# Kernel tuning notes

Hardware: AMD Instinct MI355X
Metric: run time of the kernel (lower is better)

The kernel has to match this reference:

```python
import jax, jax.numpy as jnp
import numpy as np

DIM = 256
HEADS = 8
HEAD_DIM = DIM // HEADS            # 32
EXP_HEADS = 16                     # int(2.0 * HEADS)
N = 2048
E = 32768
SCALE = HEAD_DIM ** -0.5
MASK_VALUE = -1e9  # safe stand-in for -finfo.max (avoids inf after the head-expand linear)


def setup_inputs() -> dict:
    key = jax.random.key(0)
    ks = jax.random.split(key, 9)
    s = 0.05
    return {
        "x": jax.random.normal(ks[0], (N, DIM), dtype=jnp.float32),
        "edges": jax.random.normal(ks[1], (N, DIM), dtype=jnp.float32),
        "edge_index": jax.random.randint(ks[2], (2, E), 0, N, dtype=jnp.int64),
        "Wq": jax.random.normal(ks[3], (DIM, DIM), dtype=jnp.float32) * s,
        "Wk": jax.random.normal(ks[4], (DIM, DIM), dtype=jnp.float32) * s,
        "Wv": jax.random.normal(ks[5], (EXP_HEADS * HEAD_DIM, DIM), dtype=jnp.float32) * s,
        "Wev": jax.random.normal(ks[6], (EXP_HEADS * HEAD_DIM, DIM), dtype=jnp.float32) * s,
        "Wexp": jax.random.normal(ks[7], (EXP_HEADS, HEADS), dtype=jnp.float32) * s,
        "Wout": jax.random.normal(ks[8], (DIM, EXP_HEADS * HEAD_DIM), dtype=jnp.float32) * s,
    }


def reference(x, edges, edge_index, Wq, Wk, Wv, Wev, Wexp, Wout):
    n = x.shape[0]
    # projections; torch Linear weight is (out, in) -> x @ W.T
    q = (x @ Wq.T).reshape(n, HEADS, HEAD_DIM).transpose(1, 0, 2)            # h n d
    k = (x @ Wk.T).reshape(n, HEADS, HEAD_DIM).transpose(1, 0, 2) * SCALE    # h n d
    v = (x @ Wv.T).reshape(n, EXP_HEADS, HEAD_DIM).transpose(1, 0, 2)        # e n d
    edge_v = (edges @ Wev.T).reshape(n, EXP_HEADS, HEAD_DIM).transpose(1, 0, 2)

    src, dst = edge_index[0], edge_index[1]
    # per-edge elementwise dot product: gather q at src, k at dst
    ew = jnp.einsum('hpd,hpd->hp', q[:, src], k[:, dst])                     # h E

    # scatter into dense (heads, n, n) attention, masked elsewhere
    attn = jnp.full((HEADS, n, n), MASK_VALUE, dtype=x.dtype)
    attn = attn.at[:, src, dst].set(ew)

    # head-expand linear over the head axis: (n m h) @ (exp h)^T -> exp n m
    attn = jnp.einsum('hnm,eh->enm', attn, Wexp)
    attn = jax.nn.softmax(attn, axis=-1)

    # graph Laplacian: I - A
    attn = jnp.eye(n, dtype=x.dtype)[None, :, :] - attn                      # e n m

    vv = v + edge_v                                                          # e n d
    out = jnp.einsum('enm,emd->end', attn, vv)                               # e n d
    out = out.transpose(1, 0, 2).reshape(n, EXP_HEADS * HEAD_DIM)
    out = out @ Wout.T                                                       # n dim
    return out
```

## Files before the change

kernel.cpp:

```cpp
#include <hip/hip_runtime.h>

#define NN 2048
#define DIMM 256
#define HEADS 8
#define HEAD_DIM 32
#define EXPH 16
#define E_EDGES 32768
#define VDIM 512
#define PW 1024
#define SCALE_F 0.17677669529663687f
#define MASKV -1.0e9f
#define SLOTW 64
#define CS_BLOCKS 128
#define CS_ROWS (NN / CS_BLOCKS)

typedef __attribute__((ext_vector_type(8))) short short8;
typedef __attribute__((ext_vector_type(4))) float f32x4;

__device__ __forceinline__ unsigned short f2bf(float f) {
    unsigned int u = __float_as_uint(f);
    unsigned int r = (u + 0x7FFFu + ((u >> 16) & 1u)) >> 16;
    return (unsigned short)r;
}
__device__ __forceinline__ float bflo(unsigned int u) { return __uint_as_float(u << 16); }
__device__ __forceinline__ float bfhi(unsigned int u) { return __uint_as_float(u & 0xFFFF0000u); }

__device__ __forceinline__ int load_edge(const int* __restrict__ ei32, int is64, int idx) {
    return is64 ? ei32[2 * idx] : ei32[idx];
}

__global__ __launch_bounds__(256) void convert_init_kernel(
    const float* __restrict__ x, const float* __restrict__ edges,
    const float* __restrict__ Wq, const float* __restrict__ Wk,
    const float* __restrict__ Wv, const float* __restrict__ Wev,
    const float* __restrict__ Wout,
    unsigned short* __restrict__ xb, unsigned short* __restrict__ eb,
    unsigned short* __restrict__ Wqb, unsigned short* __restrict__ Wkb,
    unsigned short* __restrict__ Wvb, unsigned short* __restrict__ Wevb,
    unsigned short* __restrict__ Woutb,
    int* __restrict__ slotCnt)
{
    int b = blockIdx.x;
    int t = threadIdx.x;
    if (b >= 1536) {
        slotCnt[(b - 1536) * 256 + t] = 0;
        return;
    }
    int idx = b * 256 + t;
    const float* src; unsigned short* dst; int loc;
    if      (idx < 131072) { src = x;     dst = xb;    loc = idx; }
    else if (idx < 262144) { src = edges; dst = eb;    loc = idx - 131072; }
    else if (idx < 278528) { src = Wq;    dst = Wqb;   loc = idx - 262144; }
    else if (idx < 294912) { src = Wk;    dst = Wkb;   loc = idx - 278528; }
    else if (idx < 327680) { src = Wv;    dst = Wvb;   loc = idx - 294912; }
    else if (idx < 360448) { src = Wev;   dst = Wevb;  loc = idx - 327680; }
    else                   { src = Wout;  dst = Woutb; loc = idx - 360448; }
    float4 v = *(const float4*)(src + (size_t)loc * 4);
    ushort4 o;
    o.x = f2bf(v.x); o.y = f2bf(v.y); o.z = f2bf(v.z); o.w = f2bf(v.w);
    *(ushort4*)(dst + (size_t)loc * 4) = o;
}

__global__ __launch_bounds__(256) void proj_mfma_kernel(
    const unsigned short* __restrict__ xb, const unsigned short* __restrict__ eb,
    const unsigned short* __restrict__ Wqb, const unsigned short* __restrict__ Wkb,
    const unsigned short* __restrict__ Wvb, const unsigned short* __restrict__ Wevb,
    unsigned short* __restrict__ Pb)
{
    int t = threadIdx.x;
    int lane = t & 63;
    int wave = t >> 6;
    int wm = wave >> 1;
    int wn = wave & 1;
    int rowT = blockIdx.x * 32;
    int jb = blockIdx.y;
    int colT = jb * 64;

    const unsigned short* Wb; int wbase; int nseg = 1;
    if (jb < 4)      { Wb = Wqb; wbase = jb * 64; }
    else if (jb < 8) { Wb = Wkb; wbase = (jb - 4) * 64; }
    else             { Wb = Wvb; wbase = (jb - 8) * 64; nseg = 2; }

    int arow = rowT + wm * 16 + (lane & 15);
    int koff = (lane >> 4) * 8;

    f32x4 acc0 = {0.f, 0.f, 0.f, 0.f};
    f32x4 acc1 = {0.f, 0.f, 0.f, 0.f};

    for (int seg = 0; seg < nseg; ++seg) {
        const unsigned short* Ab = (seg == 0) ? xb : eb;
        const unsigned short* Wm = (seg == 0) ? Wb : Wevb;
        const unsigned short* ap  = Ab + (size_t)arow * DIMM + koff;
        const unsigned short* b0p = Wm + (size_t)(wbase + wn * 32 + (lane & 15)) * DIMM + koff;
        const unsigned short* b1p = b0p + 16 * DIMM;
        #pragma unroll
        for (int ks = 0; ks < 8; ks++) {
            short8 af = *(const short8*)(ap  + ks * 32);
            short8 b0 = *(const short8*)(b0p + ks * 32);
            short8 b1 = *(const short8*)(b1p + ks * 32);
            acc0 = __builtin_amdgcn_mfma_f32_16x16x32_bf16(af, b0, acc0, 0, 0, 0);
            acc1 = __builtin_amdgcn_mfma_f32_16x16x32_bf16(af, b1, acc1, 0, 0, 0);
        }
    }
    float sc = (jb >= 4 && jb < 8) ? SCALE_F : 1.0f;
    int crow0 = rowT + wm * 16 + (lane >> 4) * 4;
    int ccol  = colT + wn * 32 + (lane & 15);
    #pragma unroll
    for (int r = 0; r < 4; r++) {
        Pb[(size_t)(crow0 + r) * PW + ccol]      = f2bf(acc0[r] * sc);
        Pb[(size_t)(crow0 + r) * PW + ccol + 16] = f2bf(acc1[r] * sc);
    }
}

__global__ __launch_bounds__(256) void colsum1_scatter_kernel(
    const unsigned short* __restrict__ Pb, float* __restrict__ partial,
    const int* __restrict__ ei32, int* __restrict__ slotCnt,
    unsigned int* __restrict__ slots)
{
    int b = blockIdx.x;
    int t = threadIdx.x;
    int nz = __syncthreads_count(ei32[2 * t + 1] != 0);
    int is64 = (nz == 0);
    int p = b * 256 + t;
    int s = load_edge(ei32, is64, p);
    int d = load_edge(ei32, is64, E_EDGES + p);
    int pos = atomicAdd(&slotCnt[s], 1);
    if (pos < SLOTW)
        slots[(size_t)s * SLOTW + pos] = (unsigned int)(p * 2048 + d);
    int r0 = b * CS_ROWS;
    float sx = 0.f, sy = 0.f;
    #pragma unroll
    for (int r = 0; r < CS_ROWS; r++) {
        unsigned int u = ((const unsigned int*)(Pb + (size_t)(r0 + r) * PW + 512))[t];
        sx += bflo(u); sy += bfhi(u);
    }
    partial[(size_t)b * VDIM + 2 * t]     = sx;
    partial[(size_t)b * VDIM + 2 * t + 1] = sy;
}

__global__ __launch_bounds__(512) void colsum2_kernel(
    const float* __restrict__ partial, float* __restrict__ colsum)
{
    int t = threadIdx.x;
    float s = 0.f;
    for (int b = 0; b < CS_BLOCKS; b++) s += partial[(size_t)b * VDIM + t];
    colsum[t] = s;
}

__global__ __launch_bounds__(256) void laplacian_kernel(
    const int* __restrict__ slotCnt, const unsigned int* __restrict__ slots,
    const float* __restrict__ Wexp, const float* __restrict__ colsum,
    const unsigned short* __restrict__ Pb, unsigned short* __restrict__ out2b)
{
    __shared__ unsigned int pkS[SLOTW], srtS[SLOTW];
    __shared__ int liveS[SLOTW];
    __shared__ float ewS[SLOTW][HEADS];
    __shared__ float aS[SLOTW][EXPH];
    __shared__ float WexpS[EXPH * HEADS];
    __shared__ float qS[DIMM];
    __shared__ float MeS[EXPH], rmaxS[EXPH], denomS[EXPH], wmaskS[EXPH];
    __shared__ int Dcnt;
    int n = blockIdx.x;
    int t = threadIdx.x;
    int cnt = slotCnt[n];
    if (cnt > SLOTW) cnt = SLOTW;
    if (t == 0) Dcnt = 0;
    if (t < EXPH * HEADS) WexpS[t] = Wexp[t];
    if (t < cnt) pkS[t] = slots[(size_t)n * SLOTW + t];
    if (t < 128) {
        unsigned int u = ((const unsigned int*)(Pb + (size_t)n * PW))[t];
        qS[2 * t]     = bflo(u);
        qS[2 * t + 1] = bfhi(u);
    }
    __syncthreads();
    if (t < cnt) {
        unsigned int pk = pkS[t];
        int rank = 0;
        for (int j = 0; j < cnt; j++) rank += (pkS[j] < pk) ? 1 : 0;
        srtS[rank] = pk;
    }
    if (t < EXPH) {
        float s = 0.f;
        #pragma unroll
        for (int h = 0; h < HEADS; h++) s += MASKV * WexpS[t * HEADS + h];
        MeS[t] = s;
    }
    __syncthreads();
    if (t < cnt) {
        unsigned int d = srtS[t] & 2047u;
        int live = 1;
        for (int j = t + 1; j < cnt; j++)
            if ((srtS[j] & 2047u) == d) { live = 0; break; }
        liveS[t] = live;
        if (live) atomicAdd(&Dcnt, 1);
    }
    {
        int h = t & 7;
        const float* qh = qS + h * 32;
        for (int i = t >> 3; i < cnt; i += 32) {
            int dsti = (int)(srtS[i] & 2047u);
            const uint4* kr = (const uint4*)(Pb + (size_t)dsti * PW + 256 + h * 32);
            float s = 0.f;
            #pragma unroll
            for (int m = 0; m < 4; m++) {
                uint4 u = kr[m];
                const float* qq = qh + m * 8;
                s += qq[0] * bflo(u.x) + qq[1] * bfhi(u.x)
                   + qq[2] * bflo(u.y) + qq[3] * bfhi(u.y)
                   + qq[4] * bflo(u.z) + qq[5] * bfhi(u.z)
                   + qq[6] * bflo(u.w) + qq[7] * bfhi(u.w);
            }
            ewS[i][h] = s;
        }
    }
    __syncthreads();
    for (int idx = t; idx < cnt * EXPH; idx += 256) {
        int i = idx >> 4, e = idx & 15;
        float a = 0.f;
        #pragma unroll
        for (int hh = 0; hh < HEADS; hh++) a += ewS[i][hh] * WexpS[e * HEADS + hh];
        aS[i][e] = a;
    }
    __syncthreads();
    if (t < EXPH) {
        int e = t;
        float rmax = MeS[e];
        for (int i = 0; i < cnt; i++) if (liveS[i]) rmax = fmaxf(rmax, aS[i][e]);
        rmaxS[e] = rmax;
    }
    __syncthreads();
    for (int idx = t; idx < cnt * EXPH; idx += 256) {
        int i = idx >> 4, e = idx & 15;
        aS[i][e] = liveS[i] ? expf(aS[i][e] - rmaxS[e]) : 0.f;
    }
    __syncthreads();
    int D = Dcnt;
    if (t < EXPH) {
        int e = t;
        float wmE = expf(MeS[e] - rmaxS[e]);
        float denom = (float)(NN - D) * wmE;
        for (int i = 0; i < cnt; i++) denom += aS[i][e];
        denomS[e] = denom;
        wmaskS[e] = wmE / denom;
    }
    __syncthreads();
    int e = t >> 4;
    float wm = wmaskS[e];
    float invD = 1.0f / denomS[e];
    unsigned int uv = ((const unsigned int*)(Pb + (size_t)n * PW + 512))[t];
    float2 cv = ((const float2*)colsum)[t];
    float ax = bflo(uv) - wm * cv.x;
    float ay = bfhi(uv) - wm * cv.y;
    for (int i = 0; i < cnt; i++) {
        if (!liveS[i]) continue;
        float w = wm - aS[i][e] * invD;
        int dsti = (int)(srtS[i] & 2047u);
        unsigned int ub = ((const unsigned int*)(Pb + (size_t)dsti * PW + 512))[t];
        ax += w * bflo(ub);
        ay += w * bfhi(ub);
    }
    unsigned int* o = (unsigned int*)(out2b + (size_t)n * VDIM);
    o[t] = (unsigned int)f2bf(ax) | ((unsigned int)f2bf(ay) << 16);
}

__global__ __launch_bounds__(256) void outgemm_mfma_kernel(
    const unsigned short* __restrict__ Ab, const unsigned short* __restrict__ Wb,
    float* __restrict__ C)
{
    int t = threadIdx.x;
    int lane = t & 63;
    int wn = t >> 6;
    int rowT = blockIdx.x * 16;
    int colT = blockIdx.y * 64 + wn * 16;

    int arow = rowT + (lane & 15);
    int koff = (lane >> 4) * 8;

    f32x4 acc = {0.f, 0.f, 0.f, 0.f};

    const unsigned short* ap = Ab + (size_t)arow * VDIM + koff;
    const unsigned short* bp = Wb + (size_t)(colT + (lane & 15)) * VDIM + koff;
    #pragma unroll
    for (int ks = 0; ks < 16; ks++) {
        short8 af = *(const short8*)(ap + ks * 32);
        short8 bf = *(const short8*)(bp + ks * 32);
        acc = __builtin_amdgcn_mfma_f32_16x16x32_bf16(af, bf, acc, 0, 0, 0);
    }
    int crow0 = rowT + (lane >> 4) * 4;
    int ccol  = colT + (lane & 15);
    #pragma unroll
    for (int r = 0; r < 4; r++)
        C[(size_t)(crow0 + r) * DIMM + ccol] = acc[r];
}

extern "C" void kernel_launch(void* const* d_in, const int* in_sizes, int n_in,
                              void* d_out, int out_size, void* d_ws, size_t ws_size,
                              hipStream_t stream) {
    const float* x     = (const float*)d_in[0];
    const float* edges = (const float*)d_in[1];
    const int*   ei32  = (const int*)d_in[2];
    const float* Wq    = (const float*)d_in[3];
    const float* Wk    = (const float*)d_in[4];
    const float* Wv    = (const float*)d_in[5];
    const float* Wev   = (const float*)d_in[6];
    const float* Wexp  = (const float*)d_in[7];
    const float* Wout  = (const float*)d_in[8];
    float* out = (float*)d_out;

    char* ws = (char*)d_ws;
    size_t off = 0;
    auto alloc = [&](size_t bytes) -> void* {
        void* p = ws + off;
        off = (off + bytes + 255) & ~(size_t)255;
        return p;
    };
    unsigned short* Pb    = (unsigned short*)alloc((size_t)NN * PW * 2);
    float* partial        = (float*)alloc((size_t)CS_BLOCKS * VDIM * 4);
    float* colsum         = (float*)alloc(VDIM * 4);
    unsigned short* xb    = (unsigned short*)alloc((size_t)NN * DIMM * 2);
    unsigned short* eb    = (unsigned short*)alloc((size_t)NN * DIMM * 2);
    unsigned short* Wqb   = (unsigned short*)alloc((size_t)DIMM * DIMM * 2);
    unsigned short* Wkb   = (unsigned short*)alloc((size_t)DIMM * DIMM * 2);
    unsigned short* Wvb   = (unsigned short*)alloc((size_t)VDIM * DIMM * 2);
    unsigned short* Wevb  = (unsigned short*)alloc((size_t)VDIM * DIMM * 2);
    unsigned short* Woutb = (unsigned short*)alloc((size_t)DIMM * VDIM * 2);
    unsigned short* out2b = (unsigned short*)alloc((size_t)NN * VDIM * 2);
    int* slotCnt          = (int*)alloc(NN * 4);
    unsigned int* slots   = (unsigned int*)alloc((size_t)NN * SLOTW * 4);
    (void)ws_size; (void)in_sizes; (void)n_in; (void)out_size;

    convert_init_kernel<<<1544, 256, 0, stream>>>(x, edges, Wq, Wk, Wv, Wev, Wout,
                                                  xb, eb, Wqb, Wkb, Wvb, Wevb, Woutb,
                                                  slotCnt);
    proj_mfma_kernel<<<dim3(64, 16), 256, 0, stream>>>(xb, eb, Wqb, Wkb, Wvb, Wevb, Pb);
    colsum1_scatter_kernel<<<CS_BLOCKS, 256, 0, stream>>>(Pb, partial, ei32, slotCnt, slots);
    colsum2_kernel<<<1, 512, 0, stream>>>(partial, colsum);
    laplacian_kernel<<<NN, 256, 0, stream>>>(slotCnt, slots, Wexp, colsum, Pb, out2b);
    outgemm_mfma_kernel<<<dim3(128, 4), 256, 0, stream>>>(out2b, Woutb, out);
}
```

Baseline: 70.50 us.

## Compute V column sums from input sums and fuse edge scatter into projection

Column sums of v+edge_v are now computed algebraically as (sum of x rows)·Wv^T + (sum of edges rows)·Wev^T. The row partial sums come from the conversion kernel and are reduced in an extra y-slice of the projection grid, which also does the edge slot scatter. This removes two kernel launches and the re-read of the projected V columns. The output GEMM also splits its K loop into two independent accumulators to expose more MFMA parallelism. The colsum now uses fp32 inputs rather than bf16-rounded projections, so values differ slightly, and 64 blocks each serially reduce 512 partials.

```diff
diff --git a/kernel.cpp b/kernel.cpp
--- a/kernel.cpp
+++ b/kernel.cpp
@@ -11,8 +11,6 @@
 #define SCALE_F 0.17677669529663687f
 #define MASKV -1.0e9f
 #define SLOTW 64
-#define CS_BLOCKS 128
-#define CS_ROWS (NN / CS_BLOCKS)
 
 typedef __attribute__((ext_vector_type(8))) short short8;
 typedef __attribute__((ext_vector_type(4))) float f32x4;
@@ -38,8 +36,10 @@
     unsigned short* __restrict__ Wqb, unsigned short* __restrict__ Wkb,
     unsigned short* __restrict__ Wvb, unsigned short* __restrict__ Wevb,
     unsigned short* __restrict__ Woutb,
+    float* __restrict__ partialX, float* __restrict__ partialE,
     int* __restrict__ slotCnt)
 {
+    __shared__ float lds[4][260];
     int b = blockIdx.x;
     int t = threadIdx.x;
     if (b >= 1536) {
@@ -59,21 +59,77 @@
     ushort4 o;
     o.x = f2bf(v.x); o.y = f2bf(v.y); o.z = f2bf(v.z); o.w = f2bf(v.w);
     *(ushort4*)(dst + (size_t)loc * 4) = o;
-}
-
-__global__ __launch_bounds__(256) void proj_mfma_kernel(
+    if (b < 1024) {
+        int lr = t >> 6;
+        int lc = (t & 63) * 4;
+        lds[lr][lc + 0] = v.x; lds[lr][lc + 1] = v.y;
+        lds[lr][lc + 2] = v.z; lds[lr][lc + 3] = v.w;
+        __syncthreads();
+        float s = lds[0][t] + lds[1][t] + lds[2][t] + lds[3][t];
+        if (b < 512) partialX[(size_t)b * 256 + t] = s;
+        else         partialE[(size_t)(b - 512) * 256 + t] = s;
+    }
+}
+
+__global__ __launch_bounds__(256) void proj_aux_kernel(
     const unsigned short* __restrict__ xb, const unsigned short* __restrict__ eb,
     const unsigned short* __restrict__ Wqb, const unsigned short* __restrict__ Wkb,
     const unsigned short* __restrict__ Wvb, const unsigned short* __restrict__ Wevb,
-    unsigned short* __restrict__ Pb)
+    unsigned short* __restrict__ Pb,
+    const int* __restrict__ ei32, int* __restrict__ slotCnt, unsigned int* __restrict__ slots,
+    const float* __restrict__ partialX, const float* __restrict__ partialE,
+    const float* __restrict__ Wv32, const float* __restrict__ Wev32,
+    float* __restrict__ colsum)
 {
+    __shared__ float xsumS[256], esumS[256], partS[8][36];
     int t = threadIdx.x;
+    int jb = blockIdx.y;
+
+    if (jb == 16) {
+        int bx = blockIdx.x;
+        int nz = __syncthreads_count(ei32[2 * t + 1] != 0);
+        int is64 = (nz == 0);
+        #pragma unroll
+        for (int r = 0; r < 2; r++) {
+            int p = bx * 512 + r * 256 + t;
+            int s = load_edge(ei32, is64, p);
+            int d = load_edge(ei32, is64, E_EDGES + p);
+            int pos = atomicAdd(&slotCnt[s], 1);
+            if (pos < SLOTW)
+                slots[(size_t)s * SLOTW + pos] = (unsigned int)(p * 2048 + d);
+        }
+        float sx = 0.f, se = 0.f;
+        for (int b2 = 0; b2 < 512; b2++) {
+            sx += partialX[(size_t)b2 * 256 + t];
+            se += partialE[(size_t)b2 * 256 + t];
+        }
+        xsumS[t] = sx;
+        esumS[t] = se;
+        __syncthreads();
+        int cl = t >> 5;
+        int c  = bx * 8 + cl;
+        int k0 = (t & 31) * 8;
+        const float* wv = Wv32  + (size_t)c * 256 + k0;
+        const float* we = Wev32 + (size_t)c * 256 + k0;
+        float s = 0.f;
+        #pragma unroll
+        for (int j = 0; j < 8; j++)
+            s += xsumS[k0 + j] * wv[j] + esumS[k0 + j] * we[j];
+        partS[cl][t & 31] = s;
+        __syncthreads();
+        if (t < 8) {
+            float acc = 0.f;
+            for (int g = 0; g < 32; g++) acc += partS[t][g];
+            colsum[bx * 8 + t] = acc;
+        }
+        return;
+    }
+
     int lane = t & 63;
     int wave = t >> 6;
     int wm = wave >> 1;
     int wn = wave & 1;
     int rowT = blockIdx.x * 32;
-    int jb = blockIdx.y;
     int colT = jb * 64;
 
     const unsigned short* Wb; int wbase; int nseg = 1;
@@ -110,41 +166,6 @@
         Pb[(size_t)(crow0 + r) * PW + ccol]      = f2bf(acc0[r] * sc);
         Pb[(size_t)(crow0 + r) * PW + ccol + 16] = f2bf(acc1[r] * sc);
     }
-}
-
-__global__ __launch_bounds__(256) void colsum1_scatter_kernel(
-    const unsigned short* __restrict__ Pb, float* __restrict__ partial,
-    const int* __restrict__ ei32, int* __restrict__ slotCnt,
-    unsigned int* __restrict__ slots)
-{
-    int b = blockIdx.x;
-    int t = threadIdx.x;
-    int nz = __syncthreads_count(ei32[2 * t + 1] != 0);
-    int is64 = (nz == 0);
-    int p = b * 256 + t;
-    int s = load_edge(ei32, is64, p);
-    int d = load_edge(ei32, is64, E_EDGES + p);
-    int pos = atomicAdd(&slotCnt[s], 1);
-    if (pos < SLOTW)
-        slots[(size_t)s * SLOTW + pos] = (unsigned int)(p * 2048 + d);
-    int r0 = b * CS_ROWS;
-    float sx = 0.f, sy = 0.f;
-    #pragma unroll
-    for (int r = 0; r < CS_ROWS; r++) {
-        unsigned int u = ((const unsigned int*)(Pb + (size_t)(r0 + r) * PW + 512))[t];
-        sx += bflo(u); sy += bfhi(u);
-    }
-    partial[(size_t)b * VDIM + 2 * t]     = sx;
-    partial[(size_t)b * VDIM + 2 * t + 1] = sy;
-}
-
-__global__ __launch_bounds__(512) void colsum2_kernel(
-    const float* __restrict__ partial, float* __restrict__ colsum)
-{
-    int t = threadIdx.x;
-    float s = 0.f;
-    for (int b = 0; b < CS_BLOCKS; b++) s += partial[(size_t)b * VDIM + t];
-    colsum[t] = s;
 }
 
 __global__ __launch_bounds__(256) void laplacian_kernel(
@@ -276,21 +297,25 @@
     int arow = rowT + (lane & 15);
     int koff = (lane >> 4) * 8;
 
-    f32x4 acc = {0.f, 0.f, 0.f, 0.f};
+    f32x4 accA = {0.f, 0.f, 0.f, 0.f};
+    f32x4 accB = {0.f, 0.f, 0.f, 0.f};
 
     const unsigned short* ap = Ab + (size_t)arow * VDIM + koff;
     const unsigned short* bp = Wb + (size_t)(colT + (lane & 15)) * VDIM + koff;
     #pragma unroll
-    for (int ks = 0; ks < 16; ks++) {
-        short8 af = *(const short8*)(ap + ks * 32);
-        short8 bf = *(const short8*)(bp + ks * 32);
-        acc = __builtin_amdgcn_mfma_f32_16x16x32_bf16(af, bf, acc, 0, 0, 0);
+    for (int ks = 0; ks < 8; ks++) {
+        short8 afA = *(const short8*)(ap + ks * 32);
+        short8 bfA = *(const short8*)(bp + ks * 32);
+        accA = __builtin_amdgcn_mfma_f32_16x16x32_bf16(afA, bfA, accA, 0, 0, 0);
+        short8 afB = *(const short8*)(ap + (ks + 8) * 32);
+        short8 bfB = *(const short8*)(bp + (ks + 8) * 32);
+        accB = __builtin_amdgcn_mfma_f32_16x16x32_bf16(afB, bfB, accB, 0, 0, 0);
     }
     int crow0 = rowT + (lane >> 4) * 4;
     int ccol  = colT + (lane & 15);
     #pragma unroll
     for (int r = 0; r < 4; r++)
-        C[(size_t)(crow0 + r) * DIMM + ccol] = acc[r];
+        C[(size_t)(crow0 + r) * DIMM + ccol] = accA[r] + accB[r];
 }
 
 extern "C" void kernel_launch(void* const* d_in, const int* in_sizes, int n_in,
@@ -315,7 +340,8 @@
         return p;
     };
     unsigned short* Pb    = (unsigned short*)alloc((size_t)NN * PW * 2);
-    float* partial        = (float*)alloc((size_t)CS_BLOCKS * VDIM * 4);
+    float* partialX       = (float*)alloc((size_t)512 * 256 * 4);
+    float* partialE       = (float*)alloc((size_t)512 * 256 * 4);
     float* colsum         = (float*)alloc(VDIM * 4);
     unsigned short* xb    = (unsigned short*)alloc((size_t)NN * DIMM * 2);
     unsigned short* eb    = (unsigned short*)alloc((size_t)NN * DIMM * 2);
@@ -331,10 +357,10 @@
 
     convert_init_kernel<<<1544, 256, 0, stream>>>(x, edges, Wq, Wk, Wv, Wev, Wout,
                                                   xb, eb, Wqb, Wkb, Wvb, Wevb, Woutb,
-                                                  slotCnt);
-    proj_mfma_kernel<<<dim3(64, 16), 256, 0, stream>>>(xb, eb, Wqb, Wkb, Wvb, Wevb, Pb);
-    colsum1_scatter_kernel<<<CS_BLOCKS, 256, 0, stream>>>(Pb, partial, ei32, slotCnt, slots);
-    colsum2_kernel<<<1, 512, 0, stream>>>(partial, colsum);
+                                                  partialX, partialE, slotCnt);
+    proj_aux_kernel<<<dim3(64, 17), 256, 0, stream>>>(xb, eb, Wqb, Wkb, Wvb, Wevb, Pb,
+                                                      ei32, slotCnt, slots,
+                                                      partialX, partialE, Wv, Wev, colsum);
     laplacian_kernel<<<NN, 256, 0, stream>>>(slotCnt, slots, Wexp, colsum, Pb, out2b);
     outgemm_mfma_kernel<<<dim3(128, 4), 256, 0, stream>>>(out2b, Woutb, out);
 }
```

New measurement: 77.02 us. 9.2% more time.
